# Optimization experiments

Hardware: AMD Instinct MI355X
Metric: run time of the kernel (lower is better)

Reference implementation:

```python
import jax, jax.numpy as jnp
import numpy as np

NUM_EXPERTS = 8
TOP_K = 2
BALANCE_LOSS_COEF = 0.01


def setup_inputs() -> dict:
    key = jax.random.key(0)
    ks = jax.random.split(key, 5)
    B, S, H, I, E = 8, 2048, 512, 2048, NUM_EXPERTS
    return {
        "hidden_states": jax.random.normal(ks[0], (B, S, H), dtype=jnp.float32),
        "Wg": jax.random.normal(ks[1], (H, E), dtype=jnp.float32) * (1.0 / np.sqrt(H)),
        "bg": jnp.zeros((E,), dtype=jnp.float32),
        "W1": jax.random.normal(ks[2], (E, H, I), dtype=jnp.float32) * (1.0 / np.sqrt(H)),
        "b1": jnp.zeros((E, I), dtype=jnp.float32),
        "W2": jax.random.normal(ks[3], (E, I, H), dtype=jnp.float32) * (1.0 / np.sqrt(I)),
        "b2": jnp.zeros((E, H), dtype=jnp.float32),
    }


def reference(hidden_states, Wg, bg, W1, b1, W2, b2):
    B, S, H = hidden_states.shape
    E, K = NUM_EXPERTS, TOP_K

    # ---- Router: softmax gate + top-k, renormalized weights ----
    logits = jnp.einsum('bsh,he->bse', hidden_states, Wg) + bg       # [B,S,E]
    probs = jax.nn.softmax(logits, axis=-1)                          # [B,S,E]
    top_p, top_i = jax.lax.top_k(probs, K)                           # [B,S,K]
    routing_weights = top_p / jnp.sum(top_p, axis=-1, keepdims=True)  # [B,S,K]

    # ---- Experts: compute every expert densely (small fixed E), then gather ----
    h = jnp.einsum('bsh,ehi->ebsi', hidden_states, W1) + b1[:, None, None, :]
    h = jax.nn.gelu(h)
    y = jnp.einsum('ebsi,eih->ebsh', h, W2) + b2[:, None, None, :]   # [E,B,S,H]

    y = jnp.moveaxis(y, 0, 2)                                        # [B,S,E,H]
    sel = jnp.take_along_axis(y, top_i[..., None], axis=2)           # [B,S,K,H]
    output = jnp.sum(routing_weights[..., None] * sel, axis=2) + hidden_states

    # ---- Load balancing loss (Switch-style): E * sum_e f_e * P_e ----
    assign = jnp.sum(jax.nn.one_hot(top_i, E, dtype=probs.dtype), axis=2)  # [B,S,E]
    f = jnp.mean(assign, axis=(0, 1)) / K                            # fraction dispatched
    P = jnp.mean(probs, axis=(0, 1))                                 # mean router prob
    balance_loss = BALANCE_LOSS_COEF * E * jnp.sum(f * P)

    return output, balance_loss
```

## Files before the change

kernel.cpp:

```cpp
#include <hip/hip_runtime.h>

#define BS_TOK 16384
#define HD 512
#define IDIM 2048
#define NE 8
#define RT_MAX 264
#define CAP (RT_MAX * 128)

typedef unsigned short u16;
typedef unsigned int u32;
typedef unsigned long long u64;
typedef __attribute__((ext_vector_type(8))) __bf16 bf16x8;
typedef __attribute__((ext_vector_type(4))) float f32x4;

__device__ __forceinline__ u16 f2bf(float f) {
  u32 u = __builtin_bit_cast(u32, f);
  u += 0x7fffu + ((u >> 16) & 1u);
  return (u16)(u >> 16);
}
__device__ __forceinline__ u16 f2bf_hw(float f) {
  u32 r;
  asm("v_cvt_pk_bf16_f32 %0, %1, %2" : "=v"(r) : "v"(f), "v"(f));
  return (u16)r;
}
__device__ __forceinline__ u32 pack2bf(float a, float b) {
  u32 r;
  asm("v_cvt_pk_bf16_f32 %0, %1, %2" : "=v"(r) : "v"(a), "v"(b));
  return r;
}
__device__ __forceinline__ float bflo(u32 u) { return __builtin_bit_cast(float, u << 16); }
__device__ __forceinline__ float bfhi(u32 u) { return __builtin_bit_cast(float, u & 0xffff0000u); }
__device__ __forceinline__ float gelu_t(float v) {
  float t = v * (-2.302558f - 0.1029474f * v * v);
  return v * __builtin_amdgcn_rcpf(1.0f + __builtin_amdgcn_exp2f(t));
}
__device__ __forceinline__ void gload16(const u16* g, u16* l) {
  __builtin_amdgcn_global_load_lds((const __attribute__((address_space(1))) u16*)g,
                                   (__attribute__((address_space(3))) u16*)l, 16, 0, 0);
}

__global__ __launch_bounds__(256) void k_transW(const float* __restrict__ W1, u16* __restrict__ W1T,
                                                const float* __restrict__ W2, u16* __restrict__ W2T) {
  __shared__ float t[64][65];
  int z = blockIdx.y;
  const float* in; u16* out; int Rin, Cin;
  if (z < NE) { in = W1; out = W1T; Rin = HD; Cin = IDIM; }
  else { in = W2; out = W2T; Rin = IDIM; Cin = HD; z -= NE; }
  size_t eb = (size_t)z * HD * IDIM;
  int tpr = Cin >> 6;
  int r0 = (blockIdx.x / tpr) << 6, c0 = (blockIdx.x % tpr) << 6;
  int tid = threadIdx.x;
  int row = tid >> 4, c4 = (tid & 15) << 2;
  #pragma unroll
  for (int i = 0; i < 4; ++i) {
    float4 v = *(const float4*)(in + eb + (size_t)(r0 + row + i * 16) * Cin + c0 + c4);
    t[row + i * 16][c4 + 0] = v.x; t[row + i * 16][c4 + 1] = v.y;
    t[row + i * 16][c4 + 2] = v.z; t[row + i * 16][c4 + 3] = v.w;
  }
  __syncthreads();
  int cc = tid >> 4, rr = (tid & 15) << 2;
  #pragma unroll
  for (int i = 0; i < 4; ++i) {
    int c = cc + i * 16;
    u32 lo = pack2bf(t[rr + 0][c], t[rr + 1][c]);
    u32 hi = pack2bf(t[rr + 2][c], t[rr + 3][c]);
    *(u32*)(out + eb + (size_t)(c0 + c) * Rin + r0 + rr)     = lo;
    *(u32*)(out + eb + (size_t)(c0 + c) * Rin + r0 + rr + 2) = hi;
  }
}

__global__ void k_router(const float* __restrict__ x, const float* __restrict__ Wg,
                         const float* __restrict__ bg, int* __restrict__ top_e,
                         float* __restrict__ top_w, u32* __restrict__ counts,
                         float* __restrict__ Psum, u16* __restrict__ xb) {
  __shared__ float wg_s[HD * 9];
  __shared__ float Pp[NE];
  __shared__ u32 cnt[NE];
  int tid = threadIdx.x;
  if (tid < NE) { Pp[tid] = 0.f; cnt[tid] = 0; }
  for (int i = tid; i < HD * NE; i += 256) wg_s[(i >> 3) * 9 + (i & 7)] = Wg[i];
  __syncthreads();
  int wv = tid >> 6, lane = tid & 63;
  int t = blockIdx.x * 4 + wv;

  const float4* xr = (const float4*)(x + (size_t)t * HD + lane * 8);
  float4 a = xr[0], b = xr[1];
  u32 p0 = pack2bf(a.x, a.y), p1 = pack2bf(a.z, a.w);
  u32 p2 = pack2bf(b.x, b.y), p3 = pack2bf(b.z, b.w);
  ((uint4*)(xb + (size_t)t * HD))[lane] = make_uint4(p0, p1, p2, p3);

  float acc[NE];
  #pragma unroll
  for (int e = 0; e < NE; ++e) acc[e] = 0.f;
  #pragma unroll
  for (int j = 0; j < 8; ++j) {
    int h = lane + 64 * j;
    float xv = x[(size_t)t * HD + h];
    const float* wrow = wg_s + h * 9;
    #pragma unroll
    for (int e = 0; e < NE; ++e) acc[e] += xv * wrow[e];
  }
  #pragma unroll
  for (int off = 32; off > 0; off >>= 1) {
    #pragma unroll
    for (int e = 0; e < NE; ++e) acc[e] += __shfl_down(acc[e], off);
  }
  if (lane == 0) {
    float lg[NE];
    #pragma unroll
    for (int e = 0; e < NE; ++e) lg[e] = acc[e] + bg[e];
    int i1 = 0; float m1 = lg[0];
    #pragma unroll
    for (int e = 1; e < NE; ++e) if (lg[e] > m1) { m1 = lg[e]; i1 = e; }
    int i2 = -1; float m2 = -1e30f;
    #pragma unroll
    for (int e = 0; e < NE; ++e) if (e != i1 && lg[e] > m2) { m2 = lg[e]; i2 = e; }
    float s = 0.f, p[NE];
    #pragma unroll
    for (int e = 0; e < NE; ++e) { p[e] = __expf(lg[e] - m1); s += p[e]; }
    float inv = 1.f / s;
    #pragma unroll
    for (int e = 0; e < NE; ++e) { p[e] *= inv; atomicAdd(&Pp[e], p[e]); }
    float denom = p[i1] + p[i2];
    top_e[2 * t] = i1; top_e[2 * t + 1] = i2;
    top_w[2 * t] = p[i1] / denom; top_w[2 * t + 1] = p[i2] / denom;
    atomicAdd(&cnt[i1], 1u); atomicAdd(&cnt[i2], 1u);
  }
  __syncthreads();
  if (tid < NE) { atomicAdd(&counts[tid], cnt[tid]); atomicAdd(&Psum[tid], Pp[tid]); }
}

__global__ void k_scatter(const int* __restrict__ top_e, const float* __restrict__ top_w,
                          const u32* __restrict__ counts, const float* __restrict__ Psum,
                          u32* __restrict__ pos_rel, int* __restrict__ perm_t,
                          float* __restrict__ perm_w, u32* __restrict__ padoff,
                          int* __restrict__ inv, float* __restrict__ out) {
  __shared__ u32 po[NE];
  if (threadIdx.x == 0) {
    u32 off = 0; float loss = 0.f;
    for (int e = 0; e < NE; ++e) {
      po[e] = off;
      off += ((counts[e] + 127u) / 128u) * 128u;
      loss += ((float)counts[e] / (float)(BS_TOK * 2)) * (Psum[e] / (float)BS_TOK);
    }
    if (blockIdx.x == 0) {
      for (int e = 0; e < NE; ++e) padoff[e] = po[e];
      padoff[NE] = off;
      out[(size_t)BS_TOK * HD] = 0.01f * (float)NE * loss;
    }
  }
  __syncthreads();
  int g = blockIdx.x * 256 + threadIdx.x;
  int e = top_e[g]; float wgt = top_w[g];
  int lane = threadIdx.x & 63;
  #pragma unroll
  for (int ee = 0; ee < NE; ++ee) {
    unsigned long long m = __ballot(e == ee);
    if (e == ee) {
      int nb = __popcll(m & ((1ull << lane) - 1ull));
      int leader = __ffsll((unsigned long long)m) - 1;
      u32 base = 0;
      if (lane == leader) base = atomicAdd(&pos_rel[ee], (u32)__popcll(m));
      base = __shfl(base, leader);
      int slot = (int)(po[ee] + base) + nb;
      perm_t[slot] = g >> 1;
      perm_w[slot] = wgt;
      inv[g] = slot;
    }
  }
}

template <int KSTEPS, int NCT, int NTOT, bool GATHER, bool ACT>
__global__ __launch_bounds__(256, 2) void k_gemm(
    const u16* __restrict__ A, int lda, const u16* __restrict__ W,
    const float* __restrict__ bias, const int* __restrict__ perm_t,
    const u32* __restrict__ padoff, u16* __restrict__ C) {
  __shared__ u16 As[2][8192], Bs[2][8192];
  int nb = gridDim.x;
  int b = blockIdx.x;
  int tile = (b & 7) * (nb >> 3) + (b >> 3);
  int rt = tile / NCT, ct = tile % NCT;
  u32 s0 = (u32)rt * 128u;
  if (s0 >= padoff[NE]) return;
  int e = 0;
  #pragma unroll
  for (int k = 1; k < NE; ++k) e += (s0 >= padoff[k]) ? 1 : 0;

  int tid = threadIdx.x;
  int wv = tid >> 6, lane = tid & 63;
  int l15 = lane & 15, lg4 = lane >> 4;
  int wr = wv >> 1, wc = wv & 1;

  int srow = tid >> 3;
  int cb = (tid & 7) * 16;
  int cbs = (cb ^ ((srow & 7) << 4)) >> 1;

  const u16* ap[4]; const u16* bp[4];
  #pragma unroll
  for (int i = 0; i < 4; ++i) {
    int r = i * 32 + srow;
    int arow = GATHER ? perm_t[s0 + r] : (int)(s0 + r);
    ap[i] = A + (size_t)arow * lda + cbs;
    bp[i] = W + ((size_t)e * NTOT + ct * 128 + r) * (KSTEPS * 64) + cbs;
  }

  int base_n = ct * 128 + wc * 64;
  f32x4 acc[4][4];
  #pragma unroll
  for (int j = 0; j < 4; ++j) {
    float bv = bias[e * NTOT + base_n + j * 16 + l15];
    #pragma unroll
    for (int i = 0; i < 4; ++i) acc[i][j] = f32x4{bv, bv, bv, bv};
  }

  #pragma unroll
  for (int i = 0; i < 4; ++i) gload16(ap[i], As[0] + tid * 8 + i * 2048);
  #pragma unroll
  for (int i = 0; i < 4; ++i) gload16(bp[i], Bs[0] + tid * 8 + i * 2048);
  #pragma unroll
  for (int i = 0; i < 4; ++i) gload16(ap[i] + 64, As[1] + tid * 8 + i * 2048);
  #pragma unroll
  for (int i = 0; i < 4; ++i) gload16(bp[i] + 64, Bs[1] + tid * 8 + i * 2048);
  asm volatile("s_waitcnt vmcnt(8)" ::: "memory");
  __builtin_amdgcn_sched_barrier(0);
  __builtin_amdgcn_s_barrier();

  for (int ks = 0; ks < KSTEPS; ++ks) {
    int cur = ks & 1;
    const u16* Ab = As[cur];
    const u16* Bb = Bs[cur];
    bf16x8 af[2][4], bf[2][4];
    #pragma unroll
    for (int kk = 0; kk < 2; ++kk) {
      #pragma unroll
      for (int f = 0; f < 4; ++f) {
        int ra = wr * 64 + f * 16 + l15;
        af[kk][f] = *(const bf16x8*)((const char*)Ab +
                    (ra * 128 + ((kk * 64 + lg4 * 16) ^ ((ra & 7) << 4))));
        int rb = wc * 64 + f * 16 + l15;
        bf[kk][f] = *(const bf16x8*)((const char*)Bb +
                    (rb * 128 + ((kk * 64 + lg4 * 16) ^ ((rb & 7) << 4))));
      }
    }
    asm volatile("s_waitcnt lgkmcnt(0)" ::: "memory");
    __builtin_amdgcn_sched_barrier(0);
    __builtin_amdgcn_s_barrier();

    if (ks + 2 < KSTEPS) {
      int k0 = (ks + 2) * 64;
      #pragma unroll
      for (int i = 0; i < 4; ++i) gload16(ap[i] + k0, As[cur] + tid * 8 + i * 2048);
      #pragma unroll
      for (int i = 0; i < 4; ++i) gload16(bp[i] + k0, Bs[cur] + tid * 8 + i * 2048);
    }

    __builtin_amdgcn_s_setprio(1);
    #pragma unroll
    for (int kk = 0; kk < 2; ++kk)
      #pragma unroll
      for (int i = 0; i < 4; ++i)
        #pragma unroll
        for (int j = 0; j < 4; ++j)
          acc[i][j] = __builtin_amdgcn_mfma_f32_16x16x32_bf16(af[kk][i], bf[kk][j], acc[i][j], 0, 0, 0);
    __builtin_amdgcn_s_setprio(0);

    if (ks + 1 < KSTEPS) {
      if (ks + 2 < KSTEPS) {
        asm volatile("s_waitcnt vmcnt(8)" ::: "memory");
      } else {
        asm volatile("s_waitcnt vmcnt(0)" ::: "memory");
      }
      __builtin_amdgcn_sched_barrier(0);
      __builtin_amdgcn_s_barrier();
    }
  }

  #pragma unroll
  for (int i = 0; i < 4; ++i) {
    u32 mrow = s0 + wr * 64 + i * 16 + lg4 * 4;
    #pragma unroll
    for (int rr = 0; rr < 4; ++rr) {
      u32 m = mrow + rr;
      #pragma unroll
      for (int j = 0; j < 4; ++j) {
        float v = acc[i][j][rr];
        if (ACT) v = gelu_t(v);
        C[(size_t)m * NTOT + base_n + j * 16 + l15] = f2bf_hw(v);
      }
    }
  }
}

__global__ void k_final(const float* __restrict__ x, const u16* __restrict__ y,
                        const int* __restrict__ inv, const float* __restrict__ top_w,
                        float* __restrict__ out) {
  int tid = threadIdx.x;
  int t = blockIdx.x * 4 + (tid >> 6);
  int lane = tid & 63;
  int s0 = inv[2 * t], s1 = inv[2 * t + 1];
  float w0 = top_w[2 * t], w1 = top_w[2 * t + 1];
  size_t xo = (size_t)t * HD + lane * 8;
  float4 a = *(const float4*)(x + xo);
  float4 b = *(const float4*)(x + xo + 4);
  uint4 ya = *(const uint4*)(y + (size_t)s0 * HD + lane * 8);
  uint4 yb = *(const uint4*)(y + (size_t)s1 * HD + lane * 8);
  float4 o0, o1;
  o0.x = a.x + w0 * bflo(ya.x) + w1 * bflo(yb.x);
  o0.y = a.y + w0 * bfhi(ya.x) + w1 * bfhi(yb.x);
  o0.z = a.z + w0 * bflo(ya.y) + w1 * bflo(yb.y);
  o0.w = a.w + w0 * bfhi(ya.y) + w1 * bfhi(yb.y);
  o1.x = b.x + w0 * bflo(ya.z) + w1 * bflo(yb.z);
  o1.y = b.y + w0 * bfhi(ya.z) + w1 * bfhi(yb.z);
  o1.z = b.z + w0 * bflo(ya.w) + w1 * bflo(yb.w);
  o1.w = b.w + w0 * bfhi(ya.w) + w1 * bfhi(yb.w);
  *(float4*)(out + xo) = o0;
  *(float4*)(out + xo + 4) = o1;
}

extern "C" void kernel_launch(void* const* d_in, const int* in_sizes, int n_in,
                              void* d_out, int out_size, void* d_ws, size_t ws_size,
                              hipStream_t stream) {
  const float* x  = (const float*)d_in[0];
  const float* Wg = (const float*)d_in[1];
  const float* bg = (const float*)d_in[2];
  const float* W1 = (const float*)d_in[3];
  const float* b1 = (const float*)d_in[4];
  const float* W2 = (const float*)d_in[5];
  const float* b2 = (const float*)d_in[6];
  float* out = (float*)d_out;

  char* w = (char*)d_ws;
  u32* counts   = (u32*)(w + 0);
  u32* pos_rel  = (u32*)(w + 32);
  float* Psum   = (float*)(w + 64);
  u32* padoff   = (u32*)(w + 96);
  int* top_e    = (int*)(w + 256);
  float* top_w  = (float*)(w + 256 + 131072);
  int* invm     = (int*)(w + 256 + 2 * 131072);
  int* perm_t   = (int*)(w + 256 + 3 * 131072);
  float* perm_w = (float*)(w + 256 + 3 * 131072 + 135168);
  u16* xb  = (u16*)(w + 663808);
  u16* W1T = (u16*)(w + 17441024);
  u16* W2T = (u16*)(w + 34218240);
  u16* h   = (u16*)(w + 50995456);
  u16* y   = (u16*)(w + 189407488);
  if (ws_size < 224010496ull) return;

  (void)hipMemsetAsync(w, 0, 663808, stream);
  k_transW<<<dim3(256, 16), 256, 0, stream>>>(W1, W1T, W2, W2T);
  k_router<<<BS_TOK / 4, 256, 0, stream>>>(x, Wg, bg, top_e, top_w, counts, Psum, xb);
  k_scatter<<<(BS_TOK * 2) / 256, 256, 0, stream>>>(top_e, top_w, counts, Psum,
                                                    pos_rel, perm_t, perm_w, padoff,
                                                    invm, out);
  k_gemm<8, 16, IDIM, true, true><<<RT_MAX * 16, 256, 0, stream>>>(
      xb, HD, W1T, b1, perm_t, padoff, h);
  k_gemm<32, 4, HD, false, false><<<RT_MAX * 4, 256, 0, stream>>>(
      h, IDIM, W2T, b2, perm_t, padoff, y);
  k_final<<<BS_TOK / 4, 256, 0, stream>>>(x, y, invm, top_w, out);
}
```

Baseline: 340.9 us.

## Fuse weight transpose with router and retile first expert GEMM to 128x256

```diff
diff --git a/kernel.cpp b/kernel.cpp
--- a/kernel.cpp
+++ b/kernel.cpp
@@ -9,7 +9,6 @@
 
 typedef unsigned short u16;
 typedef unsigned int u32;
-typedef unsigned long long u64;
 typedef __attribute__((ext_vector_type(8))) __bf16 bf16x8;
 typedef __attribute__((ext_vector_type(4))) float f32x4;
 
@@ -39,55 +38,56 @@
                                    (__attribute__((address_space(3))) u16*)l, 16, 0, 0);
 }
 
-__global__ __launch_bounds__(256) void k_transW(const float* __restrict__ W1, u16* __restrict__ W1T,
-                                                const float* __restrict__ W2, u16* __restrict__ W2T) {
+__global__ void k_prep(const float* __restrict__ W1, u16* __restrict__ W1T,
+                       const float* __restrict__ W2, u16* __restrict__ W2T,
+                       const float* __restrict__ x, const float* __restrict__ Wg,
+                       const float* __restrict__ bg, int* __restrict__ top_e,
+                       float* __restrict__ top_w, u32* __restrict__ counts,
+                       float* __restrict__ Psum, u16* __restrict__ xb) {
   __shared__ float t[64][65];
-  int z = blockIdx.y;
-  const float* in; u16* out; int Rin, Cin;
-  if (z < NE) { in = W1; out = W1T; Rin = HD; Cin = IDIM; }
-  else { in = W2; out = W2T; Rin = IDIM; Cin = HD; z -= NE; }
-  size_t eb = (size_t)z * HD * IDIM;
-  int tpr = Cin >> 6;
-  int r0 = (blockIdx.x / tpr) << 6, c0 = (blockIdx.x % tpr) << 6;
-  int tid = threadIdx.x;
-  int row = tid >> 4, c4 = (tid & 15) << 2;
-  #pragma unroll
-  for (int i = 0; i < 4; ++i) {
-    float4 v = *(const float4*)(in + eb + (size_t)(r0 + row + i * 16) * Cin + c0 + c4);
-    t[row + i * 16][c4 + 0] = v.x; t[row + i * 16][c4 + 1] = v.y;
-    t[row + i * 16][c4 + 2] = v.z; t[row + i * 16][c4 + 3] = v.w;
-  }
-  __syncthreads();
-  int cc = tid >> 4, rr = (tid & 15) << 2;
-  #pragma unroll
-  for (int i = 0; i < 4; ++i) {
-    int c = cc + i * 16;
-    u32 lo = pack2bf(t[rr + 0][c], t[rr + 1][c]);
-    u32 hi = pack2bf(t[rr + 2][c], t[rr + 3][c]);
-    *(u32*)(out + eb + (size_t)(c0 + c) * Rin + r0 + rr)     = lo;
-    *(u32*)(out + eb + (size_t)(c0 + c) * Rin + r0 + rr + 2) = hi;
-  }
-}
-
-__global__ void k_router(const float* __restrict__ x, const float* __restrict__ Wg,
-                         const float* __restrict__ bg, int* __restrict__ top_e,
-                         float* __restrict__ top_w, u32* __restrict__ counts,
-                         float* __restrict__ Psum, u16* __restrict__ xb) {
   __shared__ float wg_s[HD * 9];
   __shared__ float Pp[NE];
   __shared__ u32 cnt[NE];
+  int bid = blockIdx.x;
   int tid = threadIdx.x;
+  if (bid < 4096) {
+    int z = bid >> 8, tl = bid & 255;
+    const float* in; u16* out; int Rin, Cin;
+    if (z < NE) { in = W1; out = W1T; Rin = HD; Cin = IDIM; }
+    else { in = W2; out = W2T; Rin = IDIM; Cin = HD; z -= NE; }
+    size_t eb = (size_t)z * HD * IDIM;
+    int tpr = Cin >> 6;
+    int r0 = (tl / tpr) << 6, c0 = (tl % tpr) << 6;
+    int row = tid >> 4, c4 = (tid & 15) << 2;
+    #pragma unroll
+    for (int i = 0; i < 4; ++i) {
+      float4 v = *(const float4*)(in + eb + (size_t)(r0 + row + i * 16) * Cin + c0 + c4);
+      t[row + i * 16][c4 + 0] = v.x; t[row + i * 16][c4 + 1] = v.y;
+      t[row + i * 16][c4 + 2] = v.z; t[row + i * 16][c4 + 3] = v.w;
+    }
+    __syncthreads();
+    int cc = tid >> 4, rr = (tid & 15) << 2;
+    #pragma unroll
+    for (int i = 0; i < 4; ++i) {
+      int c = cc + i * 16;
+      u32 lo = pack2bf(t[rr + 0][c], t[rr + 1][c]);
+      u32 hi = pack2bf(t[rr + 2][c], t[rr + 3][c]);
+      *(u32*)(out + eb + (size_t)(c0 + c) * Rin + r0 + rr)     = lo;
+      *(u32*)(out + eb + (size_t)(c0 + c) * Rin + r0 + rr + 2) = hi;
+    }
+    return;
+  }
   if (tid < NE) { Pp[tid] = 0.f; cnt[tid] = 0; }
   for (int i = tid; i < HD * NE; i += 256) wg_s[(i >> 3) * 9 + (i & 7)] = Wg[i];
   __syncthreads();
   int wv = tid >> 6, lane = tid & 63;
-  int t = blockIdx.x * 4 + wv;
-
-  const float4* xr = (const float4*)(x + (size_t)t * HD + lane * 8);
+  int tk = (bid - 4096) * 4 + wv;
+
+  const float4* xr = (const float4*)(x + (size_t)tk * HD + lane * 8);
   float4 a = xr[0], b = xr[1];
   u32 p0 = pack2bf(a.x, a.y), p1 = pack2bf(a.z, a.w);
   u32 p2 = pack2bf(b.x, b.y), p3 = pack2bf(b.z, b.w);
-  ((uint4*)(xb + (size_t)t * HD))[lane] = make_uint4(p0, p1, p2, p3);
+  ((uint4*)(xb + (size_t)tk * HD))[lane] = make_uint4(p0, p1, p2, p3);
 
   float acc[NE];
   #pragma unroll
@@ -95,7 +95,7 @@
   #pragma unroll
   for (int j = 0; j < 8; ++j) {
     int h = lane + 64 * j;
-    float xv = x[(size_t)t * HD + h];
+    float xv = x[(size_t)tk * HD + h];
     const float* wrow = wg_s + h * 9;
     #pragma unroll
     for (int e = 0; e < NE; ++e) acc[e] += xv * wrow[e];
@@ -122,8 +122,8 @@
     #pragma unroll
     for (int e = 0; e < NE; ++e) { p[e] *= inv; atomicAdd(&Pp[e], p[e]); }
     float denom = p[i1] + p[i2];
-    top_e[2 * t] = i1; top_e[2 * t + 1] = i2;
-    top_w[2 * t] = p[i1] / denom; top_w[2 * t + 1] = p[i2] / denom;
+    top_e[2 * tk] = i1; top_e[2 * tk + 1] = i2;
+    top_w[2 * tk] = p[i1] / denom; top_w[2 * tk + 1] = p[i2] / denom;
     atomicAdd(&cnt[i1], 1u); atomicAdd(&cnt[i2], 1u);
   }
   __syncthreads();
@@ -133,8 +133,8 @@
 __global__ void k_scatter(const int* __restrict__ top_e, const float* __restrict__ top_w,
                           const u32* __restrict__ counts, const float* __restrict__ Psum,
                           u32* __restrict__ pos_rel, int* __restrict__ perm_t,
-                          float* __restrict__ perm_w, u32* __restrict__ padoff,
-                          int* __restrict__ inv, float* __restrict__ out) {
+                          u32* __restrict__ padoff, int* __restrict__ inv,
+                          float* __restrict__ out) {
   __shared__ u32 po[NE];
   if (threadIdx.x == 0) {
     u32 off = 0; float loss = 0.f;
@@ -164,17 +164,159 @@
       base = __shfl(base, leader);
       int slot = (int)(po[ee] + base) + nb;
       perm_t[slot] = g >> 1;
-      perm_w[slot] = wgt;
       inv[g] = slot;
     }
   }
 }
 
-template <int KSTEPS, int NCT, int NTOT, bool GATHER, bool ACT>
-__global__ __launch_bounds__(256, 2) void k_gemm(
-    const u16* __restrict__ A, int lda, const u16* __restrict__ W,
+__global__ __launch_bounds__(512, 2) void k_gemm1(
+    const u16* __restrict__ A, const u16* __restrict__ W,
     const float* __restrict__ bias, const int* __restrict__ perm_t,
     const u32* __restrict__ padoff, u16* __restrict__ C) {
+  __shared__ u16 As[2][128 * 64];
+  __shared__ u16 Bs[2][256 * 64];
+  int nb = gridDim.x;
+  int b = blockIdx.x;
+  int tile = (b & 7) * (nb >> 3) + (b >> 3);
+  int rt = tile >> 3, ct = tile & 7;
+  u32 s0 = (u32)rt * 128u;
+  if (s0 >= padoff[NE]) return;
+  int e = 0;
+  #pragma unroll
+  for (int k = 1; k < NE; ++k) e += (s0 >= padoff[k]) ? 1 : 0;
+
+  int tid = threadIdx.x;
+  int wv = tid >> 6, lane = tid & 63;
+  int l15 = lane & 15, lg4 = lane >> 4;
+  int wm = wv >> 2, wn = wv & 3;
+
+  int cb = (tid & 7) * 16;
+  const u16* ap[2]; const u16* bp[4];
+  #pragma unroll
+  for (int i = 0; i < 2; ++i) {
+    int row = (tid >> 3) + i * 64;
+    int off = (cb ^ ((row & 7) << 4)) >> 1;
+    ap[i] = A + (size_t)perm_t[s0 + row] * HD + off;
+  }
+  #pragma unroll
+  for (int i = 0; i < 4; ++i) {
+    int row = (tid >> 3) + i * 64;
+    int off = (cb ^ ((row & 7) << 4)) >> 1;
+    bp[i] = W + ((size_t)e * IDIM + ct * 256 + row) * HD + off;
+  }
+
+  int base_n = ct * 256 + wn * 64;
+  f32x4 acc[4][4];
+  #pragma unroll
+  for (int fc = 0; fc < 4; ++fc) {
+    float bv = bias[(size_t)e * IDIM + base_n + fc * 16 + l15];
+    #pragma unroll
+    for (int fr = 0; fr < 4; ++fr) acc[fr][fc] = f32x4{bv, bv, bv, bv};
+  }
+
+  #pragma unroll
+  for (int i = 0; i < 2; ++i) gload16(ap[i], As[0] + tid * 8 + i * 4096);
+  #pragma unroll
+  for (int i = 0; i < 4; ++i) gload16(bp[i], Bs[0] + tid * 8 + i * 4096);
+  asm volatile("s_waitcnt vmcnt(0)" ::: "memory");
+  __builtin_amdgcn_sched_barrier(0);
+  __builtin_amdgcn_s_barrier();
+  __builtin_amdgcn_sched_barrier(0);
+
+  for (int t = 0; t < 8; ++t) {
+    int d = t & 1;
+    const u16* Ab = As[d];
+    const u16* Bb = Bs[d];
+    u16* Ad = As[d ^ 1];
+    u16* Bd = Bs[d ^ 1];
+    int k0 = (t + 1) * 64;
+
+    bf16x8 af[2][4], bfr[2][2];
+    #pragma unroll
+    for (int kk = 0; kk < 2; ++kk) {
+      #pragma unroll
+      for (int fr = 0; fr < 4; ++fr) {
+        int ra = wm * 64 + fr * 16 + l15;
+        af[kk][fr] = *(const bf16x8*)((const char*)Ab +
+                     (ra * 128 + ((kk * 64 + lg4 * 16) ^ ((ra & 7) << 4))));
+      }
+      #pragma unroll
+      for (int q = 0; q < 2; ++q) {
+        int rb = wn * 64 + q * 16 + l15;
+        bfr[kk][q] = *(const bf16x8*)((const char*)Bb +
+                     (rb * 128 + ((kk * 64 + lg4 * 16) ^ ((rb & 7) << 4))));
+      }
+    }
+    if (t + 1 < 8) {
+      #pragma unroll
+      for (int i = 0; i < 2; ++i) gload16(ap[i] + k0, Ad + tid * 8 + i * 4096);
+      #pragma unroll
+      for (int i = 0; i < 2; ++i) gload16(bp[i] + k0, Bd + tid * 8 + i * 4096);
+    }
+    asm volatile("s_waitcnt lgkmcnt(0)" ::: "memory");
+    __builtin_amdgcn_sched_barrier(0);
+    __builtin_amdgcn_s_setprio(1);
+    #pragma unroll
+    for (int kk = 0; kk < 2; ++kk)
+      #pragma unroll
+      for (int fr = 0; fr < 4; ++fr)
+        #pragma unroll
+        for (int q = 0; q < 2; ++q)
+          acc[fr][q] = __builtin_amdgcn_mfma_f32_16x16x32_bf16(af[kk][fr], bfr[kk][q], acc[fr][q], 0, 0, 0);
+    __builtin_amdgcn_s_setprio(0);
+
+    #pragma unroll
+    for (int kk = 0; kk < 2; ++kk) {
+      #pragma unroll
+      for (int q = 0; q < 2; ++q) {
+        int rb = wn * 64 + (2 + q) * 16 + l15;
+        bfr[kk][q] = *(const bf16x8*)((const char*)Bb +
+                     (rb * 128 + ((kk * 64 + lg4 * 16) ^ ((rb & 7) << 4))));
+      }
+    }
+    if (t + 1 < 8) {
+      #pragma unroll
+      for (int i = 2; i < 4; ++i) gload16(bp[i] + k0, Bd + tid * 8 + i * 4096);
+    }
+    asm volatile("s_waitcnt lgkmcnt(0)" ::: "memory");
+    __builtin_amdgcn_sched_barrier(0);
+    __builtin_amdgcn_s_setprio(1);
+    #pragma unroll
+    for (int kk = 0; kk < 2; ++kk)
+      #pragma unroll
+      for (int fr = 0; fr < 4; ++fr)
+        #pragma unroll
+        for (int q = 0; q < 2; ++q)
+          acc[fr][2 + q] = __builtin_amdgcn_mfma_f32_16x16x32_bf16(af[kk][fr], bfr[kk][q], acc[fr][2 + q], 0, 0, 0);
+    __builtin_amdgcn_s_setprio(0);
+
+    if (t + 1 < 8) {
+      asm volatile("s_waitcnt vmcnt(0)" ::: "memory");
+      __builtin_amdgcn_sched_barrier(0);
+      __builtin_amdgcn_s_barrier();
+      __builtin_amdgcn_sched_barrier(0);
+    }
+  }
+
+  #pragma unroll
+  for (int fr = 0; fr < 4; ++fr) {
+    u32 mrow = s0 + wm * 64 + fr * 16 + lg4 * 4;
+    #pragma unroll
+    for (int rr = 0; rr < 4; ++rr) {
+      #pragma unroll
+      for (int fc = 0; fc < 4; ++fc) {
+        float v = gelu_t(acc[fr][fc][rr]);
+        C[(size_t)(mrow + rr) * IDIM + base_n + fc * 16 + l15] = f2bf_hw(v);
+      }
+    }
+  }
+}
+
+template <int KSTEPS, int NCT, int NTOT>
+__global__ __launch_bounds__(256, 2) void k_gemm2(
+    const u16* __restrict__ A, int lda, const u16* __restrict__ W,
+    const float* __restrict__ bias, const u32* __restrict__ padoff,
+    u16* __restrict__ C) {
   __shared__ u16 As[2][8192], Bs[2][8192];
   int nb = gridDim.x;
   int b = blockIdx.x;
@@ -199,8 +341,7 @@
   #pragma unroll
   for (int i = 0; i < 4; ++i) {
     int r = i * 32 + srow;
-    int arow = GATHER ? perm_t[s0 + r] : (int)(s0 + r);
-    ap[i] = A + (size_t)arow * lda + cbs;
+    ap[i] = A + (size_t)(s0 + r) * lda + cbs;
     bp[i] = W + ((size_t)e * NTOT + ct * 128 + r) * (KSTEPS * 64) + cbs;
   }
 
@@ -282,11 +423,8 @@
     for (int rr = 0; rr < 4; ++rr) {
       u32 m = mrow + rr;
       #pragma unroll
-      for (int j = 0; j < 4; ++j) {
-        float v = acc[i][j][rr];
-        if (ACT) v = gelu_t(v);
-        C[(size_t)m * NTOT + base_n + j * 16 + l15] = f2bf_hw(v);
-      }
+      for (int j = 0; j < 4; ++j)
+        C[(size_t)m * NTOT + base_n + j * 16 + l15] = f2bf_hw(acc[i][j][rr]);
     }
   }
 }
@@ -338,7 +476,6 @@
   float* top_w  = (float*)(w + 256 + 131072);
   int* invm     = (int*)(w + 256 + 2 * 131072);
   int* perm_t   = (int*)(w + 256 + 3 * 131072);
-  float* perm_w = (float*)(w + 256 + 3 * 131072 + 135168);
   u16* xb  = (u16*)(w + 663808);
   u16* W1T = (u16*)(w + 17441024);
   u16* W2T = (u16*)(w + 34218240);
@@ -347,14 +484,11 @@
   if (ws_size < 224010496ull) return;
 
   (void)hipMemsetAsync(w, 0, 663808, stream);
-  k_transW<<<dim3(256, 16), 256, 0, stream>>>(W1, W1T, W2, W2T);
-  k_router<<<BS_TOK / 4, 256, 0, stream>>>(x, Wg, bg, top_e, top_w, counts, Psum, xb);
+  k_prep<<<8192, 256, 0, stream>>>(W1, W1T, W2, W2T, x, Wg, bg,
+                                   top_e, top_w, counts, Psum, xb);
   k_scatter<<<(BS_TOK * 2) / 256, 256, 0, stream>>>(top_e, top_w, counts, Psum,
-                                                    pos_rel, perm_t, perm_w, padoff,
-                                                    invm, out);
-  k_gemm<8, 16, IDIM, true, true><<<RT_MAX * 16, 256, 0, stream>>>(
-      xb, HD, W1T, b1, perm_t, padoff, h);
-  k_gemm<32, 4, HD, false, false><<<RT_MAX * 4, 256, 0, stream>>>(
-      h, IDIM, W2T, b2, perm_t, padoff, y);
+                                                    pos_rel, perm_t, padoff, invm, out);
+  k_gemm1<<<RT_MAX * 8, 512, 0, stream>>>(xb, W1T, b1, perm_t, padoff, h);
+  k_gemm2<32, 4, HD><<<RT_MAX * 4, 256, 0, stream>>>(h, IDIM, W2T, b2, padoff, y);
   k_final<<<BS_TOK / 4, 256, 0, stream>>>(x, y, invm, top_w, out);
 }
```

Measured after the change: 360.6 us. 1.06x slower.

## Fuse weight transpose with router, scatter second GEMM output to token order

Applied to the files above, without the earlier changes.

```diff
diff --git a/kernel.cpp b/kernel.cpp
--- a/kernel.cpp
+++ b/kernel.cpp
@@ -39,55 +39,56 @@
                                    (__attribute__((address_space(3))) u16*)l, 16, 0, 0);
 }
 
-__global__ __launch_bounds__(256) void k_transW(const float* __restrict__ W1, u16* __restrict__ W1T,
-                                                const float* __restrict__ W2, u16* __restrict__ W2T) {
+__global__ void k_prep(const float* __restrict__ W1, u16* __restrict__ W1T,
+                       const float* __restrict__ W2, u16* __restrict__ W2T,
+                       const float* __restrict__ x, const float* __restrict__ Wg,
+                       const float* __restrict__ bg, int* __restrict__ top_e,
+                       float* __restrict__ top_w, u32* __restrict__ counts,
+                       float* __restrict__ Psum, u16* __restrict__ xb) {
   __shared__ float t[64][65];
-  int z = blockIdx.y;
-  const float* in; u16* out; int Rin, Cin;
-  if (z < NE) { in = W1; out = W1T; Rin = HD; Cin = IDIM; }
-  else { in = W2; out = W2T; Rin = IDIM; Cin = HD; z -= NE; }
-  size_t eb = (size_t)z * HD * IDIM;
-  int tpr = Cin >> 6;
-  int r0 = (blockIdx.x / tpr) << 6, c0 = (blockIdx.x % tpr) << 6;
-  int tid = threadIdx.x;
-  int row = tid >> 4, c4 = (tid & 15) << 2;
-  #pragma unroll
-  for (int i = 0; i < 4; ++i) {
-    float4 v = *(const float4*)(in + eb + (size_t)(r0 + row + i * 16) * Cin + c0 + c4);
-    t[row + i * 16][c4 + 0] = v.x; t[row + i * 16][c4 + 1] = v.y;
-    t[row + i * 16][c4 + 2] = v.z; t[row + i * 16][c4 + 3] = v.w;
-  }
-  __syncthreads();
-  int cc = tid >> 4, rr = (tid & 15) << 2;
-  #pragma unroll
-  for (int i = 0; i < 4; ++i) {
-    int c = cc + i * 16;
-    u32 lo = pack2bf(t[rr + 0][c], t[rr + 1][c]);
-    u32 hi = pack2bf(t[rr + 2][c], t[rr + 3][c]);
-    *(u32*)(out + eb + (size_t)(c0 + c) * Rin + r0 + rr)     = lo;
-    *(u32*)(out + eb + (size_t)(c0 + c) * Rin + r0 + rr + 2) = hi;
-  }
-}
-
-__global__ void k_router(const float* __restrict__ x, const float* __restrict__ Wg,
-                         const float* __restrict__ bg, int* __restrict__ top_e,
-                         float* __restrict__ top_w, u32* __restrict__ counts,
-                         float* __restrict__ Psum, u16* __restrict__ xb) {
   __shared__ float wg_s[HD * 9];
   __shared__ float Pp[NE];
   __shared__ u32 cnt[NE];
+  int bid = blockIdx.x;
   int tid = threadIdx.x;
+  if (bid < 4096) {
+    int z = bid >> 8, tl = bid & 255;
+    const float* in; u16* out; int Rin, Cin;
+    if (z < NE) { in = W1; out = W1T; Rin = HD; Cin = IDIM; }
+    else { in = W2; out = W2T; Rin = IDIM; Cin = HD; z -= NE; }
+    size_t eb = (size_t)z * HD * IDIM;
+    int tpr = Cin >> 6;
+    int r0 = (tl / tpr) << 6, c0 = (tl % tpr) << 6;
+    int row = tid >> 4, c4 = (tid & 15) << 2;
+    #pragma unroll
+    for (int i = 0; i < 4; ++i) {
+      float4 v = *(const float4*)(in + eb + (size_t)(r0 + row + i * 16) * Cin + c0 + c4);
+      t[row + i * 16][c4 + 0] = v.x; t[row + i * 16][c4 + 1] = v.y;
+      t[row + i * 16][c4 + 2] = v.z; t[row + i * 16][c4 + 3] = v.w;
+    }
+    __syncthreads();
+    int cc = tid >> 4, rr = (tid & 15) << 2;
+    #pragma unroll
+    for (int i = 0; i < 4; ++i) {
+      int c = cc + i * 16;
+      u32 lo = pack2bf(t[rr + 0][c], t[rr + 1][c]);
+      u32 hi = pack2bf(t[rr + 2][c], t[rr + 3][c]);
+      u64 v = (u64)lo | ((u64)hi << 32);
+      *(u64*)(out + eb + (size_t)(c0 + c) * Rin + r0 + rr) = v;
+    }
+    return;
+  }
   if (tid < NE) { Pp[tid] = 0.f; cnt[tid] = 0; }
   for (int i = tid; i < HD * NE; i += 256) wg_s[(i >> 3) * 9 + (i & 7)] = Wg[i];
   __syncthreads();
   int wv = tid >> 6, lane = tid & 63;
-  int t = blockIdx.x * 4 + wv;
-
-  const float4* xr = (const float4*)(x + (size_t)t * HD + lane * 8);
+  int tk = (bid - 4096) * 4 + wv;
+
+  const float4* xr = (const float4*)(x + (size_t)tk * HD + lane * 8);
   float4 a = xr[0], b = xr[1];
   u32 p0 = pack2bf(a.x, a.y), p1 = pack2bf(a.z, a.w);
   u32 p2 = pack2bf(b.x, b.y), p3 = pack2bf(b.z, b.w);
-  ((uint4*)(xb + (size_t)t * HD))[lane] = make_uint4(p0, p1, p2, p3);
+  ((uint4*)(xb + (size_t)tk * HD))[lane] = make_uint4(p0, p1, p2, p3);
 
   float acc[NE];
   #pragma unroll
@@ -95,7 +96,7 @@
   #pragma unroll
   for (int j = 0; j < 8; ++j) {
     int h = lane + 64 * j;
-    float xv = x[(size_t)t * HD + h];
+    float xv = x[(size_t)tk * HD + h];
     const float* wrow = wg_s + h * 9;
     #pragma unroll
     for (int e = 0; e < NE; ++e) acc[e] += xv * wrow[e];
@@ -122,8 +123,8 @@
     #pragma unroll
     for (int e = 0; e < NE; ++e) { p[e] *= inv; atomicAdd(&Pp[e], p[e]); }
     float denom = p[i1] + p[i2];
-    top_e[2 * t] = i1; top_e[2 * t + 1] = i2;
-    top_w[2 * t] = p[i1] / denom; top_w[2 * t + 1] = p[i2] / denom;
+    top_e[2 * tk] = i1; top_e[2 * tk + 1] = i2;
+    top_w[2 * tk] = p[i1] / denom; top_w[2 * tk + 1] = p[i2] / denom;
     atomicAdd(&cnt[i1], 1u); atomicAdd(&cnt[i2], 1u);
   }
   __syncthreads();
@@ -133,8 +134,7 @@
 __global__ void k_scatter(const int* __restrict__ top_e, const float* __restrict__ top_w,
                           const u32* __restrict__ counts, const float* __restrict__ Psum,
                           u32* __restrict__ pos_rel, int* __restrict__ perm_t,
-                          float* __restrict__ perm_w, u32* __restrict__ padoff,
-                          int* __restrict__ inv, float* __restrict__ out) {
+                          u32* __restrict__ padoff, float* __restrict__ out) {
   __shared__ u32 po[NE];
   if (threadIdx.x == 0) {
     u32 off = 0; float loss = 0.f;
@@ -151,7 +151,7 @@
   }
   __syncthreads();
   int g = blockIdx.x * 256 + threadIdx.x;
-  int e = top_e[g]; float wgt = top_w[g];
+  int e = top_e[g];
   int lane = threadIdx.x & 63;
   #pragma unroll
   for (int ee = 0; ee < NE; ++ee) {
@@ -163,14 +163,12 @@
       if (lane == leader) base = atomicAdd(&pos_rel[ee], (u32)__popcll(m));
       base = __shfl(base, leader);
       int slot = (int)(po[ee] + base) + nb;
-      perm_t[slot] = g >> 1;
-      perm_w[slot] = wgt;
-      inv[g] = slot;
-    }
-  }
-}
-
-template <int KSTEPS, int NCT, int NTOT, bool GATHER, bool ACT>
+      perm_t[slot] = g;
+    }
+  }
+}
+
+template <int KSTEPS, int NCT, int NTOT, bool GATHER, bool ACT, bool SCAT>
 __global__ __launch_bounds__(256, 2) void k_gemm(
     const u16* __restrict__ A, int lda, const u16* __restrict__ W,
     const float* __restrict__ bias, const int* __restrict__ perm_t,
@@ -199,7 +197,13 @@
   #pragma unroll
   for (int i = 0; i < 4; ++i) {
     int r = i * 32 + srow;
-    int arow = GATHER ? perm_t[s0 + r] : (int)(s0 + r);
+    int arow;
+    if (GATHER) {
+      int g = perm_t[s0 + r];
+      arow = (g < 0 ? 0 : g) >> 1;
+    } else {
+      arow = (int)(s0 + r);
+    }
     ap[i] = A + (size_t)arow * lda + cbs;
     bp[i] = W + ((size_t)e * NTOT + ct * 128 + r) * (KSTEPS * 64) + cbs;
   }
@@ -281,29 +285,36 @@
     #pragma unroll
     for (int rr = 0; rr < 4; ++rr) {
       u32 m = mrow + rr;
-      #pragma unroll
-      for (int j = 0; j < 4; ++j) {
-        float v = acc[i][j][rr];
-        if (ACT) v = gelu_t(v);
-        C[(size_t)m * NTOT + base_n + j * 16 + l15] = f2bf_hw(v);
+      if (SCAT) {
+        int g = perm_t[m];
+        if (g >= 0) {
+          #pragma unroll
+          for (int j = 0; j < 4; ++j)
+            C[(size_t)g * NTOT + base_n + j * 16 + l15] = f2bf_hw(acc[i][j][rr]);
+        }
+      } else {
+        #pragma unroll
+        for (int j = 0; j < 4; ++j) {
+          float v = acc[i][j][rr];
+          if (ACT) v = gelu_t(v);
+          C[(size_t)m * NTOT + base_n + j * 16 + l15] = f2bf_hw(v);
+        }
       }
     }
   }
 }
 
-__global__ void k_final(const float* __restrict__ x, const u16* __restrict__ y,
-                        const int* __restrict__ inv, const float* __restrict__ top_w,
-                        float* __restrict__ out) {
+__global__ void k_final(const float* __restrict__ x, const u16* __restrict__ y2,
+                        const float* __restrict__ top_w, float* __restrict__ out) {
   int tid = threadIdx.x;
   int t = blockIdx.x * 4 + (tid >> 6);
   int lane = tid & 63;
-  int s0 = inv[2 * t], s1 = inv[2 * t + 1];
   float w0 = top_w[2 * t], w1 = top_w[2 * t + 1];
   size_t xo = (size_t)t * HD + lane * 8;
   float4 a = *(const float4*)(x + xo);
   float4 b = *(const float4*)(x + xo + 4);
-  uint4 ya = *(const uint4*)(y + (size_t)s0 * HD + lane * 8);
-  uint4 yb = *(const uint4*)(y + (size_t)s1 * HD + lane * 8);
+  uint4 ya = *(const uint4*)(y2 + (size_t)(2 * t) * HD + lane * 8);
+  uint4 yb = *(const uint4*)(y2 + (size_t)(2 * t + 1) * HD + lane * 8);
   float4 o0, o1;
   o0.x = a.x + w0 * bflo(ya.x) + w1 * bflo(yb.x);
   o0.y = a.y + w0 * bfhi(ya.x) + w1 * bfhi(yb.x);
@@ -334,27 +345,25 @@
   u32* pos_rel  = (u32*)(w + 32);
   float* Psum   = (float*)(w + 64);
   u32* padoff   = (u32*)(w + 96);
-  int* top_e    = (int*)(w + 256);
-  float* top_w  = (float*)(w + 256 + 131072);
-  int* invm     = (int*)(w + 256 + 2 * 131072);
-  int* perm_t   = (int*)(w + 256 + 3 * 131072);
-  float* perm_w = (float*)(w + 256 + 3 * 131072 + 135168);
-  u16* xb  = (u16*)(w + 663808);
-  u16* W1T = (u16*)(w + 17441024);
-  u16* W2T = (u16*)(w + 34218240);
-  u16* h   = (u16*)(w + 50995456);
-  u16* y   = (u16*)(w + 189407488);
+  int* perm_t   = (int*)(w + 256);
+  int* top_e    = (int*)(w + 135424);
+  float* top_w  = (float*)(w + 266496);
+  u16* xb  = (u16*)(w + 397568);
+  u16* W1T = (u16*)(w + 17174784);
+  u16* W2T = (u16*)(w + 33952000);
+  u16* h   = (u16*)(w + 50729216);
+  u16* y2  = (u16*)(w + 189141248);
   if (ws_size < 224010496ull) return;
 
-  (void)hipMemsetAsync(w, 0, 663808, stream);
-  k_transW<<<dim3(256, 16), 256, 0, stream>>>(W1, W1T, W2, W2T);
-  k_router<<<BS_TOK / 4, 256, 0, stream>>>(x, Wg, bg, top_e, top_w, counts, Psum, xb);
+  (void)hipMemsetAsync(w, 0, 256, stream);
+  (void)hipMemsetAsync(w + 256, 0xFF, 135168, stream);
+  k_prep<<<8192, 256, 0, stream>>>(W1, W1T, W2, W2T, x, Wg, bg,
+                                   top_e, top_w, counts, Psum, xb);
   k_scatter<<<(BS_TOK * 2) / 256, 256, 0, stream>>>(top_e, top_w, counts, Psum,
-                                                    pos_rel, perm_t, perm_w, padoff,
-                                                    invm, out);
-  k_gemm<8, 16, IDIM, true, true><<<RT_MAX * 16, 256, 0, stream>>>(
+                                                    pos_rel, perm_t, padoff, out);
+  k_gemm<8, 16, IDIM, true, true, false><<<RT_MAX * 16, 256, 0, stream>>>(
       xb, HD, W1T, b1, perm_t, padoff, h);
-  k_gemm<32, 4, HD, false, false><<<RT_MAX * 4, 256, 0, stream>>>(
-      h, IDIM, W2T, b2, perm_t, padoff, y);
-  k_final<<<BS_TOK / 4, 256, 0, stream>>>(x, y, invm, top_w, out);
-}
+  k_gemm<32, 4, HD, false, false, true><<<RT_MAX * 4, 256, 0, stream>>>(
+      h, IDIM, W2T, b2, perm_t, padoff, y2);
+  k_final<<<BS_TOK / 4, 256, 0, stream>>>(x, y2, top_w, out);
+}
```

Result: no change. 342.2 us, median of 2 (+0.4%).
